# Kernel optimization log

Hardware: AMD Instinct MI355X
Metric: run time of the kernel (lower is better)

## Reference

```python
import jax, jax.numpy as jnp
import numpy as np

BN_EPS = 1e-5

def _resample_map(n_out):
    # out[..., i::7, j::7] = crop[..., min(i,5)::6, min(j,5)::6]
    # => output position p maps to crop position 6*(p//7) + min(p%7, 5)
    p = np.arange(n_out)
    return jnp.asarray((p // 7) * 6 + np.minimum(p % 7, 5), dtype=jnp.int32)


def setup_inputs() -> dict:
    key = jax.random.key(0)
    k = jax.random.split(key, 6)
    B, C, H, W = 32, 512, 56, 56
    C2, Cout = 2 * C, 256
    x = jax.random.normal(k[0], (B, C, H, W), dtype=jnp.float32)
    bn_gamma = jax.random.uniform(k[1], (C2,), dtype=jnp.float32, minval=0.5, maxval=1.5)
    bn_beta = jax.random.normal(k[2], (C2,), dtype=jnp.float32) * 0.1
    bn_mean = jax.random.normal(k[3], (C2,), dtype=jnp.float32) * 0.1
    bn_var = jax.random.uniform(k[4], (C2,), dtype=jnp.float32, minval=0.5, maxval=1.5)
    conv_w = jax.random.normal(k[5], (Cout, C2), dtype=jnp.float32) * (1.0 / np.sqrt(C2))
    return {"x": x, "bn_gamma": bn_gamma, "bn_beta": bn_beta,
            "bn_mean": bn_mean, "bn_var": bn_var, "conv_w": conv_w}


def reference(x, bn_gamma, bn_beta, bn_mean, bn_var, conv_w):
    # checkerboard resample: crop 56->48, expand back 48 -> 56 via separable gather
    crop = x[:, :, 4:-4, 4:-4]                      # [B,C,48,48]
    idx = _resample_map(56)                         # [56]
    up = crop[:, :, idx, :][:, :, :, idx]           # [B,C,56,56]
    cat = jnp.concatenate([x, up], axis=1)          # [B,2C,56,56]
    # origin block: BN (inference) -> ReLU -> 1x1 conv -> AvgPool 2x2 s2
    inv = (bn_gamma / jnp.sqrt(bn_var + BN_EPS))[None, :, None, None]
    h = (cat - bn_mean[None, :, None, None]) * inv + bn_beta[None, :, None, None]
    h = jax.nn.relu(h)
    y = jnp.einsum('bchw,oc->bohw', h, conv_w)      # 1x1 conv, [B,256,56,56]
    b, o, H, W = y.shape
    y = y.reshape(b, o, H // 2, 2, W // 2, 2).mean(axis=(3, 5))  # [B,256,28,28]
    return y
```

## Files before the change

kernel.cpp:

```cpp
#include <hip/hip_runtime.h>

typedef float  floatx4 __attribute__((ext_vector_type(4)));
typedef float  float4a __attribute__((ext_vector_type(4), aligned(4)));
typedef short  short8  __attribute__((ext_vector_type(8)));
typedef short  short4v __attribute__((ext_vector_type(4)));
typedef int    intx4   __attribute__((ext_vector_type(4)));

#define NB   32
#define NC   512
#define NHW  3136

template<int N> struct IC { static constexpr int value = N; };

__device__ __forceinline__ int ridx(int p) {
    int q = p / 7;
    int r = p - q * 7;
    return q * 6 + (r < 5 ? r : 5);
}
__device__ __forceinline__ short f2bf(float f) {
    unsigned int x = __builtin_bit_cast(unsigned int, f);
    x += 0x7fffu + ((x >> 16) & 1u);
    return (short)(x >> 16);
}
__device__ __forceinline__ void gload_lds16(const void* g, void* l) {
    __builtin_amdgcn_global_load_lds(
        (const __attribute__((address_space(1))) unsigned int*)g,
        (__attribute__((address_space(3))) unsigned int*)l, 16, 0, 0);
}

__global__ __launch_bounds__(256)
void prep_kernel(const float* __restrict__ w,
                 const float* __restrict__ g_, const float* __restrict__ be_,
                 const float* __restrict__ mn_, const float* __restrict__ vr_,
                 short* __restrict__ wb, float* __restrict__ pbg)
{
    int id = (blockIdx.x * 256 + threadIdx.x) * 4;
    int c  = id & 1023;
    float4a v  = *(const float4a*)(w + id);
    float4a gg = *(const float4a*)(g_ + c);
    float4a vr = *(const float4a*)(vr_ + c);
    short4v s;
#pragma unroll
    for (int j = 0; j < 4; ++j) {
        float sc = gg[j] * rsqrtf(vr[j] + 1e-5f);
        s[j] = f2bf(v[j] * sc);
    }
    *(short4v*)(wb + id) = s;
    if (blockIdx.x == 0) {
        for (int cc2 = threadIdx.x; cc2 < 1024; cc2 += 256) {
            float sc = g_[cc2] * rsqrtf(vr_[cc2] + 1e-5f);
            pbg[cc2] = be_[cc2] / sc - mn_[cc2];
        }
    }
}

__global__ __launch_bounds__(256, 2)
void fused_bn_conv_pool(const float* __restrict__ x,
                        const float* __restrict__ pbg,
                        const short* __restrict__ wgt,
                        float* __restrict__ out)
{
    __shared__ char smem[65536];
    __shared__ float pbgs[1024];
    short* WtB[2] = { (short*)(smem),         (short*)(smem + 32768) };
    short* AtB[2] = { (short*)(smem + 16384), (short*)(smem + 49152) };
    float* ys = (float*)smem;

    const int t    = threadIdx.x;
    const int bx0  = blockIdx.x;
    const int bx   = (bx0 & 7) * 224 + (bx0 >> 3);
    const int site = bx >> 1;
    const int nt   = bx & 1;
    const int b    = site / 28;
    const int ph   = site - b * 28;

    const int cc     = t & 7;
    const int mg     = t >> 3;
    const int m_base = mg * 4;
    const bool realm = (m_base < 112);
    const int rr = (m_base >= 56) ? 1 : 0;
    const int w0 = m_base - rr * 56;
    const int hs = 4 + ridx(2 * ph + rr);
    const int c0 = ridx(w0);
    const int offg = hs * 56 + 4 + c0;
    int d_[4];
#pragma unroll
    for (int j = 0; j < 4; ++j) d_[j] = ridx(w0 + j) - c0;
    const int xb   = b * NC * NHW;
    const int offd = 112 * ph + m_base;

    const int lid = t & 63;
    const int wv  = t >> 6;
    const int wo  = wv & 1;
    const int wm  = wv >> 1;
    const int col = lid & 15;
    const int q4  = lid >> 4;
    const int obw = wo * 64;
    const int mbw = wm * 64;
    const int sw  = col & 7;

    floatx4 acc[4][4];
#pragma unroll
    for (int i = 0; i < 4; ++i)
#pragma unroll
        for (int j = 0; j < 4; ++j)
            acc[i][j] = (floatx4){0.f, 0.f, 0.f, 0.f};

    const short* wrow = wgt + nt * 128 * 1024;

    *(float4a*)(pbgs + t * 4) = *(const float4a*)(pbg + t * 4);
    __syncthreads();

    float4a pf[2][8];

    auto load_into = [&](int kc, auto ic) {
        constexpr int S = decltype(ic)::value;
        if (!realm) return;
        const int k0 = kc * 64;
        const int cb = k0 + cc * 8;
        if (k0 < 512) {
#pragma unroll
            for (int i = 0; i < 8; ++i)
                pf[S][i] = *(const float4a*)(x + xb + (cb + i) * NHW + offd);
        } else {
#pragma unroll
            for (int i = 0; i < 8; ++i)
                pf[S][i] = *(const float4a*)(x + xb + (cb + i - 512) * NHW + offg);
        }
    };

    auto issue_wt = [&](int kcn, short* WtDst) {
        const int k0n = kcn * 64;
#pragma unroll
        for (int it = 0; it < 4; ++it) {
            int q = it * 256 + t;
            int o = q >> 3, sl = q & 7;
            gload_lds16(wrow + o * 1024 + k0n + ((sl ^ (o & 7)) * 8), WtDst + q * 8);
        }
    };

    auto body = [&](int kc, short* Wt, short* WtNext, short* At, auto ic, auto lastc) {
        constexpr int S    = decltype(ic)::value;
        constexpr int LAST = decltype(lastc)::value;
        const int k0 = kc * 64;
        const int cb = k0 + cc * 8;

        {
            const bool upper = (k0 >= 512);
            intx4 vj[4];
#pragma unroll
            for (int j = 0; j < 4; ++j) vj[j] = (intx4){0, 0, 0, 0};
            if (realm) {
                float4a tLo = *(const float4a*)(pbgs + cb);
                float4a tHi = *(const float4a*)(pbgs + cb + 4);
                float rprev[4];
#pragma unroll
                for (int i = 0; i < 8; ++i) {
                    const float tch = (i < 4) ? tLo[i] : tHi[i - 4];
                    float vv[4];
                    if (!upper) {
#pragma unroll
                        for (int j = 0; j < 4; ++j) vv[j] = pf[S][i][j];
                    } else {
#pragma unroll
                        for (int j = 0; j < 4; ++j) {
                            int dd = d_[j];
                            float a  = (dd >= 2) ? pf[S][i][2] : pf[S][i][0];
                            float bq = (dd >= 2) ? pf[S][i][3] : pf[S][i][1];
                            vv[j] = (dd & 1) ? bq : a;
                        }
                    }
                    if (!(i & 1)) {
#pragma unroll
                        for (int j = 0; j < 4; ++j) rprev[j] = fmaxf(vv[j] + tch, 0.f);
                    } else {
#pragma unroll
                        for (int j = 0; j < 4; ++j) {
                            float rc = fmaxf(vv[j] + tch, 0.f);
                            unsigned pk;
                            asm("v_cvt_pk_bf16_f32 %0, %1, %2"
                                : "=v"(pk) : "v"(rprev[j]), "v"(rc));
                            vj[j][i >> 1] = (int)pk;
                        }
                    }
                }
            }
#pragma unroll
            for (int j = 0; j < 4; ++j) {
                int m = m_base + j;
                *(intx4*)(At + m * 64 + ((cc ^ (m & 7)) * 8)) = vj[j];
            }
        }

        if (LAST) { asm volatile("s_waitcnt vmcnt(0)" ::: "memory"); }
        else      { asm volatile("s_waitcnt vmcnt(8)" ::: "memory"); }
        asm volatile("s_waitcnt lgkmcnt(0)" ::: "memory");
        __builtin_amdgcn_sched_barrier(0);
        __builtin_amdgcn_s_barrier();
        __builtin_amdgcn_sched_barrier(0);

        if (kc < 15) issue_wt(kc + 1, WtNext);
        __builtin_amdgcn_sched_barrier(0);
        if (kc < 14) load_into(kc + 2, ic);

        __builtin_amdgcn_s_setprio(1);
#pragma unroll
        for (int ks = 0; ks < 2; ++ks) {
            const int cb2 = ks * 4 + q4;
            short8 af[4], bf[4];
#pragma unroll
            for (int of = 0; of < 4; ++of) {
                int row = obw + of * 16 + col;
                af[of] = *(const short8*)(Wt + row * 64 + ((cb2 ^ sw) * 8));
            }
#pragma unroll
            for (int mf = 0; mf < 4; ++mf) {
                int row = mbw + mf * 16 + col;
                bf[mf] = *(const short8*)(At + row * 64 + ((cb2 ^ sw) * 8));
            }
#pragma unroll
            for (int of = 0; of < 4; ++of)
#pragma unroll
                for (int mf = 0; mf < 4; ++mf)
                    acc[of][mf] = __builtin_amdgcn_mfma_f32_16x16x32_bf16(
                        af[of], bf[mf], acc[of][mf], 0, 0, 0);
        }
        __builtin_amdgcn_s_setprio(0);
    };

    issue_wt(0, WtB[0]);
    __builtin_amdgcn_sched_barrier(0);
    load_into(0, IC<0>{});
    load_into(1, IC<1>{});

    for (int kc2 = 0; kc2 < 14; kc2 += 2) {
        body(kc2,     WtB[0], WtB[1], AtB[0], IC<0>{}, IC<0>{});
        body(kc2 + 1, WtB[1], WtB[0], AtB[1], IC<1>{}, IC<0>{});
    }
    body(14, WtB[0], WtB[1], AtB[0], IC<0>{}, IC<0>{});
    body(15, WtB[1], WtB[0], AtB[1], IC<1>{}, IC<1>{});

    __syncthreads();

#pragma unroll
    for (int s = 0; s < 4; ++s) {
        if (wo == (s >> 1)) {
#pragma unroll
            for (int of2 = 0; of2 < 2; ++of2) {
                const int of  = (s & 1) * 2 + of2;
                const int olb = of2 * 16 + q4 * 4;
#pragma unroll
                for (int mf = 0; mf < 4; ++mf) {
                    const int m = mbw + mf * 16 + col;
#pragma unroll
                    for (int rg = 0; rg < 4; ++rg)
                        ys[(olb + rg) * 132 + m] = acc[of][mf][rg];
                }
            }
        }
        __syncthreads();
        for (int i = t; i < 896; i += 256) {
            int ol = i / 28;
            int pw = i - ol * 28;
            const float* yr = ys + ol * 132 + 2 * pw;
            float v = (yr[0] + yr[1] + yr[56] + yr[57]) * 0.25f;
            int og = nt * 128 + s * 32 + ol;
            out[((b * 256 + og) * 28 + ph) * 28 + pw] = v;
        }
        __syncthreads();
    }
}

extern "C" void kernel_launch(void* const* d_in, const int* in_sizes, int n_in,
                              void* d_out, int out_size, void* d_ws, size_t ws_size,
                              hipStream_t stream) {
    (void)in_sizes; (void)n_in; (void)out_size; (void)ws_size;
    const float* x  = (const float*)d_in[0];
    const float* g  = (const float*)d_in[1];
    const float* be = (const float*)d_in[2];
    const float* mn = (const float*)d_in[3];
    const float* vr = (const float*)d_in[4];
    const float* w  = (const float*)d_in[5];
    float* o   = (float*)d_out;
    short* wb  = (short*)d_ws;
    float* pbg = (float*)((char*)d_ws + 524288);

    prep_kernel<<<dim3(256), dim3(256), 0, stream>>>(w, g, be, mn, vr, wb, pbg);
    fused_bn_conv_pool<<<dim3(32 * 28 * 2), dim3(256), 0, stream>>>(x, pbg, wb, o);
}
```

Baseline: 430.3 us.

## Pool BN-ReLU activations before the 1x1 conv, then run a smaller GEMM

Computes BN+ReLU and the 2x2 average pool first, in a separate kernel that writes a pooled bf16 activation buffer. A separate GEMM kernel then does the 1x1 conv on a quarter of the spatial positions. This reduces matrix-multiply work by a factor of four by commuting the linear pool with the linear conv. It adds an intermediate workspace buffer and an extra kernel launch. The old fused kernel is kept as a fallback when the workspace is too small.

```diff
diff --git a/kernel.cpp b/kernel.cpp
--- a/kernel.cpp
+++ b/kernel.cpp
@@ -2,6 +2,7 @@
 
 typedef float  floatx4 __attribute__((ext_vector_type(4)));
 typedef float  float4a __attribute__((ext_vector_type(4), aligned(4)));
+typedef float  float2a __attribute__((ext_vector_type(2), aligned(8)));
 typedef short  short8  __attribute__((ext_vector_type(8)));
 typedef short  short4v __attribute__((ext_vector_type(4)));
 typedef int    intx4   __attribute__((ext_vector_type(4)));
@@ -54,6 +55,177 @@
     }
 }
 
+
+__global__ __launch_bounds__(448)
+void prepool_kernel(const float* __restrict__ x,
+                    const float* __restrict__ pbg,
+                    short* __restrict__ hp)
+{
+    __shared__ float pbgs[1024];
+    const int t = threadIdx.x;
+    if (t < 256) *(float4a*)(pbgs + t * 4) = *(const float4a*)(pbg + t * 4);
+    __syncthreads();
+
+    const int bx0 = blockIdx.x;
+    const int bx  = (bx0 & 7) * 112 + (bx0 >> 3);
+    const int b   = bx / 28;
+    const int ph  = bx - b * 28;
+
+    const int pw  = t % 28;
+    const int cog = t / 28;
+
+    const int r0 = 2 * ph, r1 = 2 * ph + 1;
+    const int g0 = 4 + ridx(2 * ph);
+    const int g1 = 4 + ridx(2 * ph + 1);
+    const int cw0 = 4 + ridx(2 * pw);
+    const int d   = (4 + ridx(2 * pw + 1)) - cw0;
+    const int ew  = cw0 & ~1;
+    const int q0  = cw0 & 1;
+
+    const int m     = b * 784 + ph * 28 + pw;
+    const int xbase = b * NC * NHW;
+
+#pragma unroll
+    for (int it = 0; it < 4; ++it) {
+        const int co = it * 16 + cog;
+        float la[8], ua[8];
+#pragma unroll
+        for (int i = 0; i < 8; ++i) {
+            const float* xc = x + xbase + (co * 8 + i) * NHW;
+            float2a l0 = *(const float2a*)(xc + r0 * 56 + 2 * pw);
+            float2a l1 = *(const float2a*)(xc + r1 * 56 + 2 * pw);
+            float2a a0 = *(const float2a*)(xc + g0 * 56 + ew);
+            float2a b0 = *(const float2a*)(xc + g0 * 56 + ew + 2);
+            float2a a1 = *(const float2a*)(xc + g1 * 56 + ew);
+            float2a b1 = *(const float2a*)(xc + g1 * 56 + ew + 2);
+            float tl = pbgs[co * 8 + i];
+            float tu = pbgs[512 + co * 8 + i];
+            la[i] = 0.25f * (fmaxf(l0[0] + tl, 0.f) + fmaxf(l0[1] + tl, 0.f)
+                           + fmaxf(l1[0] + tl, 0.f) + fmaxf(l1[1] + tl, 0.f));
+            float u00 = q0 ? a0[1] : a0[0];
+            float u10 = q0 ? a1[1] : a1[0];
+            int   i1  = q0 + d;
+            float u01 = (i1 == 2) ? b0[0] : (i1 ? a0[1] : a0[0]);
+            float u11 = (i1 == 2) ? b1[0] : (i1 ? a1[1] : a1[0]);
+            ua[i] = 0.25f * (fmaxf(u00 + tu, 0.f) + fmaxf(u01 + tu, 0.f)
+                           + fmaxf(u10 + tu, 0.f) + fmaxf(u11 + tu, 0.f));
+        }
+        unsigned pl[4], pu[4];
+#pragma unroll
+        for (int j = 0; j < 4; ++j) {
+            asm("v_cvt_pk_bf16_f32 %0, %1, %2" : "=v"(pl[j]) : "v"(la[2*j]), "v"(la[2*j+1]));
+            asm("v_cvt_pk_bf16_f32 %0, %1, %2" : "=v"(pu[j]) : "v"(ua[2*j]), "v"(ua[2*j+1]));
+        }
+        *(intx4*)(hp + (co * 25088 + m) * 8) =
+            (intx4){(int)pl[0], (int)pl[1], (int)pl[2], (int)pl[3]};
+        *(intx4*)(hp + ((64 + co) * 25088 + m) * 8) =
+            (intx4){(int)pu[0], (int)pu[1], (int)pu[2], (int)pu[3]};
+    }
+}
+
+__global__ __launch_bounds__(256, 2)
+void gemm_kernel(const short* __restrict__ hp,
+                 const short* __restrict__ wgt,
+                 float* __restrict__ out)
+{
+    __shared__ char smem[65536];
+
+    const int t   = threadIdx.x;
+    const int bx0 = blockIdx.x;
+    const int bx  = (bx0 & 7) * 49 + (bx0 >> 3);
+    const int mt  = bx >> 1;
+    const int nt  = bx & 1;
+
+    const int lid = t & 63;
+    const int wv  = t >> 6;
+    const int wo  = wv & 1;
+    const int wm  = wv >> 1;
+    const int col = lid & 15;
+    const int q4  = lid >> 4;
+    const int obw = wo * 64;
+    const int mbw = wm * 64;
+    const int sw  = col & 7;
+
+    const short* wrow = wgt + nt * 128 * 1024;
+
+    floatx4 acc[4][4];
+#pragma unroll
+    for (int i = 0; i < 4; ++i)
+#pragma unroll
+        for (int j = 0; j < 4; ++j)
+            acc[i][j] = (floatx4){0.f, 0.f, 0.f, 0.f};
+
+    auto issue = [&](int kc) {
+        const int k0  = kc * 64;
+        short* Wt = (short*)(smem + (kc & 1) * 32768);
+        short* At = (short*)(smem + 16384 + (kc & 1) * 32768);
+#pragma unroll
+        for (int it = 0; it < 4; ++it) {
+            int q = it * 256 + t;
+            int o = q >> 3, sl = q & 7;
+            gload_lds16(wrow + o * 1024 + k0 + ((sl ^ (o & 7)) * 8), Wt + q * 8);
+        }
+#pragma unroll
+        for (int it = 0; it < 4; ++it) {
+            int q = it * 256 + t;
+            int m = q >> 3, sl = q & 7;
+            int cog = (k0 >> 3) + (sl ^ (m & 7));
+            gload_lds16(hp + (cog * 25088 + (mt * 128 + m)) * 8, At + q * 8);
+        }
+    };
+
+    issue(0);
+
+    for (int kc = 0; kc < 16; ++kc) {
+        asm volatile("s_waitcnt vmcnt(0)" ::: "memory");
+        __builtin_amdgcn_sched_barrier(0);
+        __builtin_amdgcn_s_barrier();
+        __builtin_amdgcn_sched_barrier(0);
+        if (kc < 15) issue(kc + 1);
+        __builtin_amdgcn_sched_barrier(0);
+
+        short* Wt = (short*)(smem + (kc & 1) * 32768);
+        short* At = (short*)(smem + 16384 + (kc & 1) * 32768);
+        __builtin_amdgcn_s_setprio(1);
+#pragma unroll
+        for (int ks = 0; ks < 2; ++ks) {
+            const int cb2 = ks * 4 + q4;
+            short8 af[4], bf[4];
+#pragma unroll
+            for (int of = 0; of < 4; ++of) {
+                int row = obw + of * 16 + col;
+                af[of] = *(const short8*)(Wt + row * 64 + ((cb2 ^ sw) * 8));
+            }
+#pragma unroll
+            for (int mf = 0; mf < 4; ++mf) {
+                int row = mbw + mf * 16 + col;
+                bf[mf] = *(const short8*)(At + row * 64 + ((cb2 ^ sw) * 8));
+            }
+#pragma unroll
+            for (int of = 0; of < 4; ++of)
+#pragma unroll
+                for (int mf = 0; mf < 4; ++mf)
+                    acc[of][mf] = __builtin_amdgcn_mfma_f32_16x16x32_bf16(
+                        af[of], bf[mf], acc[of][mf], 0, 0, 0);
+        }
+        __builtin_amdgcn_s_setprio(0);
+    }
+
+#pragma unroll
+    for (int mf = 0; mf < 4; ++mf) {
+        const int m_g = mt * 128 + mbw + mf * 16 + col;
+        const int bo  = m_g / 784;
+        const int r   = m_g - bo * 784;
+#pragma unroll
+        for (int of = 0; of < 4; ++of) {
+            const int o0 = nt * 128 + obw + of * 16 + q4 * 4;
+#pragma unroll
+            for (int rg = 0; rg < 4; ++rg)
+                out[(bo * 256 + o0 + rg) * 784 + r] = acc[of][mf][rg];
+        }
+    }
+}
+
 __global__ __launch_bounds__(256, 2)
 void fused_bn_conv_pool(const float* __restrict__ x,
                         const float* __restrict__ pbg,
@@ -144,7 +316,6 @@
         constexpr int LAST = decltype(lastc)::value;
         const int k0 = kc * 64;
         const int cb = k0 + cc * 8;
-
         {
             const bool upper = (k0 >= 512);
             intx4 vj[4];
@@ -274,7 +445,7 @@
 extern "C" void kernel_launch(void* const* d_in, const int* in_sizes, int n_in,
                               void* d_out, int out_size, void* d_ws, size_t ws_size,
                               hipStream_t stream) {
-    (void)in_sizes; (void)n_in; (void)out_size; (void)ws_size;
+    (void)in_sizes; (void)n_in; (void)out_size;
     const float* x  = (const float*)d_in[0];
     const float* g  = (const float*)d_in[1];
     const float* be = (const float*)d_in[2];
@@ -282,9 +453,22 @@
     const float* vr = (const float*)d_in[4];
     const float* w  = (const float*)d_in[5];
     float* o   = (float*)d_out;
-    short* wb  = (short*)d_ws;
-    float* pbg = (float*)((char*)d_ws + 524288);
-
-    prep_kernel<<<dim3(256), dim3(256), 0, stream>>>(w, g, be, mn, vr, wb, pbg);
-    fused_bn_conv_pool<<<dim3(32 * 28 * 2), dim3(256), 0, stream>>>(x, pbg, wb, o);
-}
+
+    const size_t HP_BYTES = 128u * 25088u * 8u * 2u;
+    const size_t WB_BYTES = 524288;
+    const size_t NEED     = HP_BYTES + WB_BYTES + 4096;
+
+    if (ws_size >= NEED) {
+        short* hp  = (short*)d_ws;
+        short* wb  = (short*)((char*)d_ws + HP_BYTES);
+        float* pbg = (float*)((char*)d_ws + HP_BYTES + WB_BYTES);
+        prep_kernel<<<dim3(256), dim3(256), 0, stream>>>(w, g, be, mn, vr, wb, pbg);
+        prepool_kernel<<<dim3(32 * 28), dim3(448), 0, stream>>>(x, pbg, hp);
+        gemm_kernel<<<dim3(196 * 2), dim3(256), 0, stream>>>(hp, wb, o);
+    } else {
+        short* wb  = (short*)d_ws;
+        float* pbg = (float*)((char*)d_ws + WB_BYTES);
+        prep_kernel<<<dim3(256), dim3(256), 0, stream>>>(w, g, be, mn, vr, wb, pbg);
+        fused_bn_conv_pool<<<dim3(32 * 28 * 2), dim3(256), 0, stream>>>(x, pbg, wb, o);
+    }
+}
```

Result: faster. 344.3 us (-20.0%).
